# Kernel tuning notes

Measured on AMD Instinct MI355X. Metric: run time of the kernel, lower is better.

Reference implementation:

```python
import jax, jax.numpy as jnp
import numpy as np

SEQ, B, D_IN, D_TRAJ, D_LSTM = 640, 40, 8, 32, 64
NH, DH = 4, 48  # n_head, att_out
EMB = NH * DH  # 192


def setup_inputs() -> dict:
    key = jax.random.key(0)
    ks = jax.random.split(key, 16)
    g = lambda k, shape: (jax.random.normal(k, shape, dtype=jnp.float32) * 0.05)
    z = lambda n: jnp.zeros((n,), jnp.float32)
    return {
        "hist": jax.random.normal(ks[0], (128, 5, 40, D_IN), dtype=jnp.float32),
        "adj": jnp.zeros((B, B), dtype=jnp.int32),  # unused (use_spatial=False)
        "W1": g(ks[1], (D_TRAJ, D_IN)), "b1": z(D_TRAJ),
        "W_ih": g(ks[2], (4 * D_LSTM, D_TRAJ)), "W_hh": g(ks[3], (4 * D_LSTM, D_LSTM)),
        "b_ih": z(4 * D_LSTM), "b_hh": z(4 * D_LSTM),
        "Wq": g(ks[4], (EMB, D_LSTM)), "bq": z(EMB),
        "Wk": g(ks[5], (EMB, D_LSTM)), "bk": z(EMB),
        "Wv": g(ks[6], (EMB, D_LSTM)), "bv": z(EMB),
        "Wa": g(ks[7], (D_LSTM, EMB)), "ba": z(D_LSTM),
        "Wg": g(ks[8], (D_LSTM, EMB)), "bg": z(D_LSTM),
        "gamma": jnp.ones((D_LSTM,), jnp.float32), "beta": z(D_LSTM),
    }


def reference(hist, adj, W1, b1, W_ih, W_hh, b_ih, b_hh,
              Wq, bq, Wk, bk, Wv, bv, Wa, ba, Wg, bg, gamma, beta):
    # trajectory embedding + ELU
    x = jax.nn.elu(jnp.einsum('...f,hf->...h', hist, W1) + b1)
    x = x.reshape(SEQ, B, D_TRAJ)  # hardcoded (128*5, 40, 32) in the module

    # single-layer LSTM (torch gate order i, f, g, o), seq-first
    def step(carry, xt):
        h, c = carry
        gates = xt @ W_ih.T + h @ W_hh.T + b_ih + b_hh
        i, f, g_, o = jnp.split(gates, 4, axis=-1)
        c = jax.nn.sigmoid(f) * c + jax.nn.sigmoid(i) * jnp.tanh(g_)
        h = jax.nn.sigmoid(o) * jnp.tanh(c)
        return (h, c), h

    h0 = jnp.zeros((B, D_LSTM), x.dtype)
    (_, _), seq = jax.lax.scan(step, (h0, h0), x)  # (640, 40, 64)

    # multi-head attention over the 40-agent axis, per time step
    def heads(W, b):
        y = seq @ W.T + b  # (640, 40, 192)
        return y.reshape(SEQ, B, NH, DH).transpose(2, 0, 1, 3)  # (4, 640, 40, 48)

    q, k, v = heads(Wq, bq), heads(Wk, bk), heads(Wv, bv)
    a = jax.nn.softmax(jnp.einsum('hnqd,hnkd->hnqk', q, k) / 8.0, axis=-1)  # /sqrt(64)
    o = jnp.einsum('hnqk,hnkd->hnqd', a, v)  # (4, 640, 40, 48)
    o = o.transpose(1, 2, 0, 3).reshape(SEQ, B, EMB)  # recombine heads -> (640, 40, 192)

    # GLU (dropout rate = 0)
    tv = (o @ Wa.T + ba) * jax.nn.sigmoid(o @ Wg.T + bg)  # (640, 40, 64)

    # Add & LayerNorm (residual with LSTM output)
    y = seq + tv
    mu = y.mean(-1, keepdims=True)
    var = ((y - mu) ** 2).mean(-1, keepdims=True)
    return (y - mu) / jnp.sqrt(var + 1e-5) * gamma + beta
```

## Files before the change

kernel.cpp:

```cpp
#include <hip/hip_runtime.h>

#define SEQ 640
#define BATCH 40
#define D_IN 8
#define D_TRAJ 32
#define D_LSTM 64
#define G4 256
#define NH 4
#define DH 48
#define EMB 192

typedef float v2f __attribute__((ext_vector_type(2)));
typedef float v4f __attribute__((ext_vector_type(4)));
typedef _Float16 h2t __attribute__((ext_vector_type(2)));

__device__ __forceinline__ float sigmoid_f(float x) {
    float e = __expf(-x);
    return __builtin_amdgcn_rcpf(1.f + e);
}
__device__ __forceinline__ float tanh_f(float x) {
    float e = __expf(2.f * x);
    return 1.f - 2.f * __builtin_amdgcn_rcpf(e + 1.f);
}

__global__ void __launch_bounds__(256) k_embed(
    const float* __restrict__ hist, const float* __restrict__ W1,
    const float* __restrict__ b1, const float* __restrict__ W_ih,
    const float* __restrict__ b_ih, const float* __restrict__ b_hh,
    float* __restrict__ gates_x)
{
    __shared__ float sh_hist[BATCH * D_IN];
    __shared__ float sh_traj[BATCH * D_TRAJ];
    const int t = blockIdx.x, tid = threadIdx.x;

    for (int i = tid; i < BATCH * D_IN; i += 256)
        sh_hist[i] = hist[t * BATCH * D_IN + i];
    __syncthreads();

    for (int idx = tid; idx < BATCH * D_TRAJ; idx += 256) {
        int b = idx >> 5, h = idx & 31;
        float acc = b1[h];
        #pragma unroll
        for (int f = 0; f < D_IN; ++f)
            acc += sh_hist[b * D_IN + f] * W1[h * D_IN + f];
        sh_traj[idx] = acc > 0.f ? acc : (__expf(acc) - 1.f);
    }
    __syncthreads();

    float w[D_TRAJ];
    #pragma unroll
    for (int h = 0; h < D_TRAJ; ++h) w[h] = W_ih[tid * D_TRAJ + h];
    const float bias = b_ih[tid] + b_hh[tid];
    const int j = tid & 63, g = tid >> 6;

    for (int b = 0; b < BATCH; ++b) {
        float acc = bias;
        #pragma unroll
        for (int h = 0; h < D_TRAJ; ++h)
            acc += sh_traj[b * D_TRAJ + h] * w[h];
        gates_x[((size_t)b * SEQ + t) * G4 + j * 4 + g] = acc;
    }
}

__global__ void __launch_bounds__(64, 1) k_lstm(
    const float* __restrict__ gates_x, const float* __restrict__ W_hh,
    float* __restrict__ seq_out)
{
    const int b = blockIdx.x, j = threadIdx.x;

    h2t wi2[32], wf2[32], wg2[32], wo2[32];
    const float* Wi = W_hh + (0 * 64 + j) * D_LSTM;
    const float* Wf = W_hh + (1 * 64 + j) * D_LSTM;
    const float* Wg = W_hh + (2 * 64 + j) * D_LSTM;
    const float* Wo = W_hh + (3 * 64 + j) * D_LSTM;
    #pragma unroll
    for (int m = 0; m < 32; ++m) {
        wi2[m] = (h2t){(_Float16)Wi[2 * m], (_Float16)Wi[2 * m + 1]};
        wf2[m] = (h2t){(_Float16)Wf[2 * m], (_Float16)Wf[2 * m + 1]};
        wg2[m] = (h2t){(_Float16)Wg[2 * m], (_Float16)Wg[2 * m + 1]};
        wo2[m] = (h2t){(_Float16)Wo[2 * m], (_Float16)Wo[2 * m + 1]};
    }

    const v4f* gxp = (const v4f*)(gates_x + (size_t)b * SEQ * G4);
    v4f g0 = gxp[0 * 64 + j];
    v4f g1 = gxp[1 * 64 + j];
    v4f g2 = gxp[2 * 64 + j];
    v4f g3 = gxp[3 * 64 + j];

    float h = 0.f, c = 0.f;
    float hpf = 0.f;

    auto lstm_step = [&](v4f& gk, int t) {
        const int hbits = __builtin_bit_cast(int, hpf);

        float ai0 = gk.x, af0 = gk.y, ag0 = gk.z, ao0 = gk.w;
        float ai1 = 0.f, af1 = 0.f, ag1 = 0.f, ao1 = 0.f;
        #pragma unroll
        for (int m = 0; m < 16; ++m) {
            int pmi = __builtin_amdgcn_readlane(hbits, 2 * m);
            h2t p = __builtin_bit_cast(h2t, pmi);
            ai0 = __builtin_amdgcn_fdot2(wi2[m], p, ai0, false);
            af0 = __builtin_amdgcn_fdot2(wf2[m], p, af0, false);
            ag0 = __builtin_amdgcn_fdot2(wg2[m], p, ag0, false);
            ao0 = __builtin_amdgcn_fdot2(wo2[m], p, ao0, false);
        }
        #pragma unroll
        for (int m = 16; m < 32; ++m) {
            int pmi = __builtin_amdgcn_readlane(hbits, 2 * m);
            h2t p = __builtin_bit_cast(h2t, pmi);
            ai1 = __builtin_amdgcn_fdot2(wi2[m], p, ai1, false);
            af1 = __builtin_amdgcn_fdot2(wf2[m], p, af1, false);
            ag1 = __builtin_amdgcn_fdot2(wg2[m], p, ag1, false);
            ao1 = __builtin_amdgcn_fdot2(wo2[m], p, ao1, false);
        }
        float ai = ai0 + ai1, af = af0 + af1, ag = ag0 + ag1, ao = ao0 + ao1;

        c = sigmoid_f(af) * c + sigmoid_f(ai) * tanh_f(ag);
        h = sigmoid_f(ao) * tanh_f(c);
        seq_out[(size_t)(t * BATCH + b) * D_LSTM + j] = h;

        float hn = __shfl_xor(h, 1, 64);
        float lo = (j & 1) ? hn : h;
        float hi = (j & 1) ? h : hn;
        h2t hpk = {(_Float16)lo, (_Float16)hi};
        hpf = __builtin_bit_cast(float, hpk);

        int tp = t + 4; if (tp > SEQ - 1) tp = SEQ - 1;
        gk = gxp[(size_t)tp * 64 + j];
    };

    for (int t = 0; t < SEQ; t += 4) {
        lstm_step(g0, t + 0);
        lstm_step(g1, t + 1);
        lstm_step(g2, t + 2);
        lstm_step(g3, t + 3);
    }
}

__global__ void __launch_bounds__(256) k_wtrans(
    const float* __restrict__ Wq, const float* __restrict__ bq,
    const float* __restrict__ Wk, const float* __restrict__ bk,
    const float* __restrict__ Wv, const float* __restrict__ bv,
    float* __restrict__ WT, float* __restrict__ bqkv)
{
    int idx = blockIdx.x * 256 + threadIdx.x;
    if (idx < 576 * 64) {
        int k = idx / 576, c = idx % 576;
        float v;
        if (c < 192)      v = Wq[c * 64 + k];
        else if (c < 384) v = Wk[(c - 192) * 64 + k];
        else              v = Wv[(c - 384) * 64 + k];
        WT[idx] = v;
    }
    if (idx < 576) {
        float v;
        if (idx < 192)      v = bq[idx];
        else if (idx < 384) v = bk[idx - 192];
        else                v = bv[idx - 384];
        bqkv[idx] = v;
    }
}

#define QKVS 584
#define SXS 68
#define SSS 44
__global__ void __launch_bounds__(256) k_attn(
    const float* __restrict__ seq, const float* __restrict__ WT,
    const float* __restrict__ bqkv, float* __restrict__ o_buf)
{
    const int t = blockIdx.x, tid = threadIdx.x;
    __shared__ _Float16 sqkv[BATCH * QKVS];
    __shared__ float sX[BATCH * SXS];

    for (int i = tid; i < BATCH * D_LSTM; i += 256)
        sX[(i >> 6) * SXS + (i & 63)] = seq[(size_t)t * BATCH * D_LSTM + i];
    __syncthreads();

    const int c0 = tid, c1 = tid + 256, c2 = tid + 512;
    const float b0v = bqkv[c0], b1v = bqkv[c1];
    const float b2v = (tid < 64) ? bqkv[c2] : 0.f;

    for (int grp = 0; grp < 2; ++grp) {
        float a0[20], a1[20], a2[20];
        #pragma unroll
        for (int r = 0; r < 20; ++r) { a0[r] = b0v; a1[r] = b1v; a2[r] = b2v; }

        for (int kq = 0; kq < 16; ++kq) {
            float w0[4], w1[4], w2[4];
            #pragma unroll
            for (int u = 0; u < 4; ++u) {
                int k = 4 * kq + u;
                w0[u] = WT[k * 576 + c0];
                w1[u] = WT[k * 576 + c1];
                w2[u] = (tid < 64) ? WT[k * 576 + c2] : 0.f;
            }
            #pragma unroll
            for (int r = 0; r < 20; ++r) {
                v4f x = *(const v4f*)&sX[(grp * 20 + r) * SXS + 4 * kq];
                a0[r] += x.x * w0[0] + x.y * w0[1] + x.z * w0[2] + x.w * w0[3];
                a1[r] += x.x * w1[0] + x.y * w1[1] + x.z * w1[2] + x.w * w1[3];
                a2[r] += x.x * w2[0] + x.y * w2[1] + x.z * w2[2] + x.w * w2[3];
            }
        }
        for (int r = 0; r < 20; ++r) {
            int bb = grp * 20 + r;
            sqkv[bb * QKVS + c0] = (_Float16)a0[r];
            sqkv[bb * QKVS + c1] = (_Float16)a1[r];
            if (tid < 64) sqkv[bb * QKVS + c2] = (_Float16)a2[r];
        }
    }
    __syncthreads();

    float* ss = sX;

    for (int h = 0; h < NH; ++h) {
        for (int p = 0; p < 2; ++p) {
            if (tid < 200) {
                int slot = p * 200 + tid;
                int i = slot / 10, jg = slot % 10;
                const v4f* qp = (const v4f*)&sqkv[i * QKVS + h * DH];
                v4f q[6];
                #pragma unroll
                for (int u = 0; u < 6; ++u) q[u] = qp[u];
                #pragma unroll
                for (int v = 0; v < 4; ++v) {
                    int jj = jg * 4 + v;
                    const v4f* kp = (const v4f*)&sqkv[jj * QKVS + 192 + h * DH];
                    float acc = 0.f;
                    #pragma unroll
                    for (int u = 0; u < 6; ++u) {
                        v4f kv = kp[u];
                        acc = __builtin_amdgcn_fdot2(
                            __builtin_bit_cast(h2t, q[u].x),
                            __builtin_bit_cast(h2t, kv.x), acc, false);
                        acc = __builtin_amdgcn_fdot2(
                            __builtin_bit_cast(h2t, q[u].y),
                            __builtin_bit_cast(h2t, kv.y), acc, false);
                        acc = __builtin_amdgcn_fdot2(
                            __builtin_bit_cast(h2t, q[u].z),
                            __builtin_bit_cast(h2t, kv.z), acc, false);
                        acc = __builtin_amdgcn_fdot2(
                            __builtin_bit_cast(h2t, q[u].w),
                            __builtin_bit_cast(h2t, kv.w), acc, false);
                    }
                    ss[i * SSS + jj] = acc * 0.125f;
                }
            }
        }
        __syncthreads();

        if (tid < BATCH) {
            v4f* rp = (v4f*)&ss[tid * SSS];
            v4f r[10];
            #pragma unroll
            for (int u = 0; u < 10; ++u) r[u] = rp[u];
            float m = -1e30f;
            #pragma unroll
            for (int u = 0; u < 10; ++u)
                m = fmaxf(m, fmaxf(fmaxf(r[u].x, r[u].y), fmaxf(r[u].z, r[u].w)));
            float s = 0.f;
            #pragma unroll
            for (int u = 0; u < 10; ++u) {
                r[u].x = __expf(r[u].x - m); s += r[u].x;
                r[u].y = __expf(r[u].y - m); s += r[u].y;
                r[u].z = __expf(r[u].z - m); s += r[u].z;
                r[u].w = __expf(r[u].w - m); s += r[u].w;
            }
            float inv = __builtin_amdgcn_rcpf(s);
            #pragma unroll
            for (int u = 0; u < 10; ++u) {
                r[u].x *= inv; r[u].y *= inv; r[u].z *= inv; r[u].w *= inv;
                rp[u] = r[u];
            }
        }
        __syncthreads();

        if (tid < 240) {
            int bi = tid / 6, dg = tid % 6, d0 = dg * 8;
            const v4f* sp = (const v4f*)&ss[bi * SSS];
            v4f sr[10];
            #pragma unroll
            for (int u = 0; u < 10; ++u) sr[u] = sp[u];
            float acc[8];
            #pragma unroll
            for (int d = 0; d < 8; ++d) acc[d] = 0.f;
            for (int jj = 0; jj < 40; ++jj) {
                float a = ((const float*)&sr[jj >> 2])[jj & 3];
                v4f vv = *(const v4f*)&sqkv[jj * QKVS + 384 + h * DH + d0];
                #pragma unroll
                for (int w = 0; w < 4; ++w) {
                    h2t pr = __builtin_bit_cast(h2t, ((const float*)&vv)[w]);
                    acc[2 * w]     += a * (float)pr[0];
                    acc[2 * w + 1] += a * (float)pr[1];
                }
            }
            float* ob = &o_buf[((size_t)t * BATCH + bi) * EMB + h * DH + d0];
            #pragma unroll
            for (int d = 0; d < 8; ++d) ob[d] = acc[d];
        }
        __syncthreads();
    }
}

__global__ void __launch_bounds__(256) k_glu_ln(
    const float* __restrict__ seq, const float* __restrict__ obuf,
    const float* __restrict__ Wa, const float* __restrict__ ba,
    const float* __restrict__ Wg, const float* __restrict__ bg,
    const float* __restrict__ gamma, const float* __restrict__ beta,
    float* __restrict__ out)
{
    const int t = blockIdx.x, tid = threadIdx.x;
    __shared__ float so[BATCH * 193];
    __shared__ float sy[BATCH * 65];
    __shared__ float sseq[BATCH * D_LSTM];

    const float* ot = obuf + (size_t)t * BATCH * EMB;
    for (int i = tid; i < BATCH * EMB; i += 256)
        so[(i / EMB) * 193 + (i % EMB)] = ot[i];
    for (int i = tid; i < BATCH * D_LSTM; i += 256)
        sseq[i] = seq[(size_t)t * BATCH * D_LSTM + i];
    __syncthreads();

    const int j = tid >> 2, bgr = tid & 3;
    float acc_a[10], acc_g[10];
    #pragma unroll
    for (int bb = 0; bb < 10; ++bb) { acc_a[bb] = ba[j]; acc_g[bb] = bg[j]; }

    const float* wa = Wa + j * EMB;
    const float* wg = Wg + j * EMB;
    for (int p = 0; p < EMB; ++p) {
        float a = wa[p], g = wg[p];
        #pragma unroll
        for (int bb = 0; bb < 10; ++bb) {
            float o = so[(bgr + 4 * bb) * 193 + p];
            acc_a[bb] += o * a;
            acc_g[bb] += o * g;
        }
    }
    #pragma unroll
    for (int bb = 0; bb < 10; ++bb) {
        int b = bgr + 4 * bb;
        float tv = acc_a[bb] * sigmoid_f(acc_g[bb]);
        sy[b * 65 + j] = sseq[b * D_LSTM + j] + tv;
    }
    __syncthreads();

    const int w = tid >> 6, lane = tid & 63;
    const float gm = gamma[lane], bt = beta[lane];
    for (int rr = 0; rr < 10; ++rr) {
        int b = w + 4 * rr;
        float y = sy[b * 65 + lane];
        float s1 = y, s2 = y * y;
        #pragma unroll
        for (int m = 1; m < 64; m <<= 1) {
            s1 += __shfl_xor(s1, m, 64);
            s2 += __shfl_xor(s2, m, 64);
        }
        float mu  = s1 * (1.f / 64.f);
        float var = s2 * (1.f / 64.f) - mu * mu;
        float inv = rsqrtf(var + 1e-5f);
        out[(size_t)t * BATCH * D_LSTM + b * D_LSTM + lane] = (y - mu) * inv * gm + bt;
    }
}

extern "C" void kernel_launch(void* const* d_in, const int* in_sizes, int n_in,
                              void* d_out, int out_size, void* d_ws, size_t ws_size,
                              hipStream_t stream)
{
    const float* hist = (const float*)d_in[0];
    const float* W1   = (const float*)d_in[2];
    const float* b1   = (const float*)d_in[3];
    const float* W_ih = (const float*)d_in[4];
    const float* W_hh = (const float*)d_in[5];
    const float* b_ih = (const float*)d_in[6];
    const float* b_hh = (const float*)d_in[7];
    const float* Wq   = (const float*)d_in[8];
    const float* bq   = (const float*)d_in[9];
    const float* Wk   = (const float*)d_in[10];
    const float* bk   = (const float*)d_in[11];
    const float* Wv   = (const float*)d_in[12];
    const float* bv   = (const float*)d_in[13];
    const float* Wa   = (const float*)d_in[14];
    const float* ba   = (const float*)d_in[15];
    const float* Wg   = (const float*)d_in[16];
    const float* bg   = (const float*)d_in[17];
    const float* gamma = (const float*)d_in[18];
    const float* beta  = (const float*)d_in[19];
    float* out = (float*)d_out;

    float* ws = (float*)d_ws;
    float* gates_x = ws;
    float* seq     = ws + 6553600;
    float* obuf    = ws + 6553600 + 1638400;
    float* WT      = ws + 6553600 + 1638400 + 4915200;
    float* bqkv    = WT + 36864;

    hipLaunchKernelGGL(k_wtrans, dim3(144), dim3(256), 0, stream,
                       Wq, bq, Wk, bk, Wv, bv, WT, bqkv);
    hipLaunchKernelGGL(k_embed, dim3(SEQ), dim3(256), 0, stream,
                       hist, W1, b1, W_ih, b_ih, b_hh, gates_x);
    hipLaunchKernelGGL(k_lstm, dim3(BATCH), dim3(64), 0, stream,
                       gates_x, W_hh, seq);
    hipLaunchKernelGGL(k_attn, dim3(SEQ), dim3(256), 0, stream,
                       seq, WT, bqkv, obuf);
    hipLaunchKernelGGL(k_glu_ln, dim3(SEQ), dim3(256), 0, stream,
                       seq, obuf, Wa, ba, Wg, bg, gamma, beta, out);
}
```

Before: 513.1 us.

## Fuse attention with GLU+LayerNorm and use DPP for LSTM hidden-state exchange

Merges the attention and GLU/LayerNorm kernels so each head's output stays in shared memory and is folded into GLU accumulators right away, which removes the o_buf global round trip and one launch. The LSTM's recurrent h exchange swaps a shuffle for a DPP quad-permute of packed fp16 halves, shortening the serial per-step critical path. W_ih loads in the embed kernel become vectorized. The cost is more registers and shared memory in the fused kernel, which may lower occupancy, and the LSTM chain is still the dominant serial part.

```diff
diff --git a/kernel.cpp b/kernel.cpp
--- a/kernel.cpp
+++ b/kernel.cpp
@@ -48,8 +48,14 @@
     __syncthreads();
 
     float w[D_TRAJ];
-    #pragma unroll
-    for (int h = 0; h < D_TRAJ; ++h) w[h] = W_ih[tid * D_TRAJ + h];
+    {
+        const v4f* wv = (const v4f*)(W_ih + tid * D_TRAJ);
+        #pragma unroll
+        for (int u = 0; u < 8; ++u) {
+            v4f x = wv[u];
+            w[4*u] = x.x; w[4*u+1] = x.y; w[4*u+2] = x.z; w[4*u+3] = x.w;
+        }
+    }
     const float bias = b_ih[tid] + b_hh[tid];
     const int j = tid & 63, g = tid >> 6;
 
@@ -89,6 +95,7 @@
 
     float h = 0.f, c = 0.f;
     float hpf = 0.f;
+    const bool odd = (j & 1);
 
     auto lstm_step = [&](v4f& gk, int t) {
         const int hbits = __builtin_bit_cast(int, hpf);
@@ -119,11 +126,10 @@
         h = sigmoid_f(ao) * tanh_f(c);
         seq_out[(size_t)(t * BATCH + b) * D_LSTM + j] = h;
 
-        float hn = __shfl_xor(h, 1, 64);
-        float lo = (j & 1) ? hn : h;
-        float hi = (j & 1) ? h : hn;
-        h2t hpk = {(_Float16)lo, (_Float16)hi};
-        hpf = __builtin_bit_cast(float, hpk);
+        int own = (int)__builtin_bit_cast(unsigned short, (_Float16)h);
+        int nb  = __builtin_amdgcn_update_dpp(0, own, 0xB1, 0xF, 0xF, true);
+        int pk  = odd ? (nb | (own << 16)) : (own | (nb << 16));
+        hpf = __builtin_bit_cast(float, pk);
 
         int tp = t + 4; if (tp > SEQ - 1) tp = SEQ - 1;
         gk = gxp[(size_t)tp * 64 + j];
@@ -164,13 +170,18 @@
 #define QKVS 584
 #define SXS 68
 #define SSS 44
-__global__ void __launch_bounds__(256) k_attn(
+#define SOS 52
+__global__ void __launch_bounds__(256, 2) k_attn_glu(
     const float* __restrict__ seq, const float* __restrict__ WT,
-    const float* __restrict__ bqkv, float* __restrict__ o_buf)
+    const float* __restrict__ bqkv,
+    const float* __restrict__ Wa, const float* __restrict__ ba,
+    const float* __restrict__ Wg, const float* __restrict__ bg,
+    const float* __restrict__ gamma, const float* __restrict__ beta,
+    float* __restrict__ out)
 {
     const int t = blockIdx.x, tid = threadIdx.x;
     __shared__ _Float16 sqkv[BATCH * QKVS];
-    __shared__ float sX[BATCH * SXS];
+    __shared__ float sX[5280];
 
     for (int i = tid; i < BATCH * D_LSTM; i += 256)
         sX[(i >> 6) * SXS + (i & 63)] = seq[(size_t)t * BATCH * D_LSTM + i];
@@ -212,6 +223,12 @@
     __syncthreads();
 
     float* ss = sX;
+    float* so = sX + 2720;
+
+    const int gj = tid >> 2, bgr = tid & 3;
+    float acc_a[10], acc_g[10];
+    #pragma unroll
+    for (int bb = 0; bb < 10; ++bb) { acc_a[bb] = ba[gj]; acc_g[bb] = bg[gj]; }
 
     for (int h = 0; h < NH; ++h) {
         for (int p = 0; p < 2; ++p) {
@@ -294,72 +311,58 @@
                     acc[2 * w + 1] += a * (float)pr[1];
                 }
             }
-            float* ob = &o_buf[((size_t)t * BATCH + bi) * EMB + h * DH + d0];
-            #pragma unroll
-            for (int d = 0; d < 8; ++d) ob[d] = acc[d];
+            v4f* op = (v4f*)&so[bi * SOS + d0];
+            op[0] = (v4f){acc[0], acc[1], acc[2], acc[3]};
+            op[1] = (v4f){acc[4], acc[5], acc[6], acc[7]};
         }
         __syncthreads();
-    }
-}
-
-__global__ void __launch_bounds__(256) k_glu_ln(
-    const float* __restrict__ seq, const float* __restrict__ obuf,
-    const float* __restrict__ Wa, const float* __restrict__ ba,
-    const float* __restrict__ Wg, const float* __restrict__ bg,
-    const float* __restrict__ gamma, const float* __restrict__ beta,
-    float* __restrict__ out)
-{
-    const int t = blockIdx.x, tid = threadIdx.x;
-    __shared__ float so[BATCH * 193];
-    __shared__ float sy[BATCH * 65];
-    __shared__ float sseq[BATCH * D_LSTM];
-
-    const float* ot = obuf + (size_t)t * BATCH * EMB;
-    for (int i = tid; i < BATCH * EMB; i += 256)
-        so[(i / EMB) * 193 + (i % EMB)] = ot[i];
+
+        {
+            const v4f* wap = (const v4f*)(Wa + gj * EMB + h * DH);
+            const v4f* wgp = (const v4f*)(Wg + gj * EMB + h * DH);
+            for (int pc = 0; pc < 12; ++pc) {
+                v4f a4 = wap[pc], g4 = wgp[pc];
+                #pragma unroll
+                for (int bb = 0; bb < 10; ++bb) {
+                    v4f ov = *(const v4f*)&so[(bgr + 4 * bb) * SOS + 4 * pc];
+                    acc_a[bb] += ov.x * a4.x + ov.y * a4.y + ov.z * a4.z + ov.w * a4.w;
+                    acc_g[bb] += ov.x * g4.x + ov.y * g4.y + ov.z * g4.z + ov.w * g4.w;
+                }
+            }
+        }
+    }
+
     for (int i = tid; i < BATCH * D_LSTM; i += 256)
-        sseq[i] = seq[(size_t)t * BATCH * D_LSTM + i];
-    __syncthreads();
-
-    const int j = tid >> 2, bgr = tid & 3;
-    float acc_a[10], acc_g[10];
-    #pragma unroll
-    for (int bb = 0; bb < 10; ++bb) { acc_a[bb] = ba[j]; acc_g[bb] = bg[j]; }
-
-    const float* wa = Wa + j * EMB;
-    const float* wg = Wg + j * EMB;
-    for (int p = 0; p < EMB; ++p) {
-        float a = wa[p], g = wg[p];
-        #pragma unroll
-        for (int bb = 0; bb < 10; ++bb) {
-            float o = so[(bgr + 4 * bb) * 193 + p];
-            acc_a[bb] += o * a;
-            acc_g[bb] += o * g;
-        }
-    }
+        sX[i] = seq[(size_t)t * BATCH * D_LSTM + i];
+    __syncthreads();
+
+    float* sy = sX + 2680;
     #pragma unroll
     for (int bb = 0; bb < 10; ++bb) {
         int b = bgr + 4 * bb;
         float tv = acc_a[bb] * sigmoid_f(acc_g[bb]);
-        sy[b * 65 + j] = sseq[b * D_LSTM + j] + tv;
-    }
-    __syncthreads();
-
-    const int w = tid >> 6, lane = tid & 63;
-    const float gm = gamma[lane], bt = beta[lane];
-    for (int rr = 0; rr < 10; ++rr) {
-        int b = w + 4 * rr;
-        float y = sy[b * 65 + lane];
-        float s1 = y, s2 = y * y;
-        #pragma unroll
-        for (int m = 1; m < 64; m <<= 1) {
-            s1 += __shfl_xor(s1, m, 64);
-            s2 += __shfl_xor(s2, m, 64);
-        }
-        float mu  = s1 * (1.f / 64.f);
-        float var = s2 * (1.f / 64.f) - mu * mu;
-        float inv = rsqrtf(var + 1e-5f);
-        out[(size_t)t * BATCH * D_LSTM + b * D_LSTM + lane] = (y - mu) * inv * gm + bt;
+        sy[b * 65 + gj] = sX[b * D_LSTM + gj] + tv;
+    }
+    __syncthreads();
+
+    {
+        const int w = tid >> 6, lane = tid & 63;
+        const float gm = gamma[lane], bt = beta[lane];
+        for (int rr = 0; rr < 10; ++rr) {
+            int b = w + 4 * rr;
+            float y = sy[b * 65 + lane];
+            float s1 = y, s2 = y * y;
+            #pragma unroll
+            for (int m = 1; m < 64; m <<= 1) {
+                s1 += __shfl_xor(s1, m, 64);
+                s2 += __shfl_xor(s2, m, 64);
+            }
+            float mu  = s1 * (1.f / 64.f);
+            float var = s2 * (1.f / 64.f) - mu * mu;
+            float inv = rsqrtf(var + 1e-5f);
+            out[(size_t)t * BATCH * D_LSTM + b * D_LSTM + lane] =
+                (y - mu) * inv * gm + bt;
+        }
     }
 }
 
@@ -391,8 +394,7 @@
     float* ws = (float*)d_ws;
     float* gates_x = ws;
     float* seq     = ws + 6553600;
-    float* obuf    = ws + 6553600 + 1638400;
-    float* WT      = ws + 6553600 + 1638400 + 4915200;
+    float* WT      = ws + 6553600 + 1638400;
     float* bqkv    = WT + 36864;
 
     hipLaunchKernelGGL(k_wtrans, dim3(144), dim3(256), 0, stream,
@@ -401,8 +403,6 @@
                        hist, W1, b1, W_ih, b_ih, b_hh, gates_x);
     hipLaunchKernelGGL(k_lstm, dim3(BATCH), dim3(64), 0, stream,
                        gates_x, W_hh, seq);
-    hipLaunchKernelGGL(k_attn, dim3(SEQ), dim3(256), 0, stream,
-                       seq, WT, bqkv, obuf);
-    hipLaunchKernelGGL(k_glu_ln, dim3(SEQ), dim3(256), 0, stream,
-                       seq, obuf, Wa, ba, Wg, bg, gamma, beta, out);
-}
+    hipLaunchKernelGGL(k_attn_glu, dim3(SEQ), dim3(256), 0, stream,
+                       seq, WT, bqkv, Wa, ba, Wg, bg, gamma, beta, out);
+}
```

Result: faster. 502.6 us (-2.1%).

## Split attention per head across blocks, drop weight-transpose kernel, use DPP in LSTM

Applied to the files above, without the earlier changes.

The attention kernel now launches one block per (head, timestep) instead of one per timestep. Each block computes only its head's Q/K/V projection, with 144 threads each holding a 64-wide weight row in registers loaded straight from the original weights. This removes the separate transpose kernel and the serial per-head loop, and gives four times more blocks. The cost is that the seq tile is loaded four times and 112 threads sit idle during projection. The LSTM neighbour exchange swaps a shuffle for a DPP quad-permute on packed fp16 bits, and the embed kernel loads W_ih with vector loads.

```diff
diff --git a/kernel.cpp b/kernel.cpp
--- a/kernel.cpp
+++ b/kernel.cpp
@@ -48,8 +48,14 @@
     __syncthreads();
 
     float w[D_TRAJ];
-    #pragma unroll
-    for (int h = 0; h < D_TRAJ; ++h) w[h] = W_ih[tid * D_TRAJ + h];
+    {
+        const v4f* wv = (const v4f*)(W_ih + tid * D_TRAJ);
+        #pragma unroll
+        for (int u = 0; u < 8; ++u) {
+            v4f x = wv[u];
+            w[4*u] = x.x; w[4*u+1] = x.y; w[4*u+2] = x.z; w[4*u+3] = x.w;
+        }
+    }
     const float bias = b_ih[tid] + b_hh[tid];
     const int j = tid & 63, g = tid >> 6;
 
@@ -89,6 +95,7 @@
 
     float h = 0.f, c = 0.f;
     float hpf = 0.f;
+    const bool odd = (j & 1);
 
     auto lstm_step = [&](v4f& gk, int t) {
         const int hbits = __builtin_bit_cast(int, hpf);
@@ -119,11 +126,10 @@
         h = sigmoid_f(ao) * tanh_f(c);
         seq_out[(size_t)(t * BATCH + b) * D_LSTM + j] = h;
 
-        float hn = __shfl_xor(h, 1, 64);
-        float lo = (j & 1) ? hn : h;
-        float hi = (j & 1) ? h : hn;
-        h2t hpk = {(_Float16)lo, (_Float16)hi};
-        hpf = __builtin_bit_cast(float, hpk);
+        int own = (int)__builtin_bit_cast(unsigned short, (_Float16)h);
+        int nb  = __builtin_amdgcn_update_dpp(0, own, 0xB1, 0xF, 0xF, true);
+        int pk  = odd ? (nb | (own << 16)) : (own | (nb << 16));
+        hpf = __builtin_bit_cast(float, pk);
 
         int tp = t + 4; if (tp > SEQ - 1) tp = SEQ - 1;
         gk = gxp[(size_t)tp * 64 + j];
@@ -137,168 +143,125 @@
     }
 }
 
-__global__ void __launch_bounds__(256) k_wtrans(
+#define SAS 68
+#define SKVS 152
+#define SSS 44
+__global__ void __launch_bounds__(256) k_attn(
+    const float* __restrict__ seq,
     const float* __restrict__ Wq, const float* __restrict__ bq,
     const float* __restrict__ Wk, const float* __restrict__ bk,
     const float* __restrict__ Wv, const float* __restrict__ bv,
-    float* __restrict__ WT, float* __restrict__ bqkv)
-{
-    int idx = blockIdx.x * 256 + threadIdx.x;
-    if (idx < 576 * 64) {
-        int k = idx / 576, c = idx % 576;
-        float v;
-        if (c < 192)      v = Wq[c * 64 + k];
-        else if (c < 384) v = Wk[(c - 192) * 64 + k];
-        else              v = Wv[(c - 384) * 64 + k];
-        WT[idx] = v;
-    }
-    if (idx < 576) {
-        float v;
-        if (idx < 192)      v = bq[idx];
-        else if (idx < 384) v = bk[idx - 192];
-        else                v = bv[idx - 384];
-        bqkv[idx] = v;
-    }
-}
-
-#define QKVS 584
-#define SXS 68
-#define SSS 44
-__global__ void __launch_bounds__(256) k_attn(
-    const float* __restrict__ seq, const float* __restrict__ WT,
-    const float* __restrict__ bqkv, float* __restrict__ o_buf)
-{
-    const int t = blockIdx.x, tid = threadIdx.x;
-    __shared__ _Float16 sqkv[BATCH * QKVS];
-    __shared__ float sX[BATCH * SXS];
+    float* __restrict__ o_buf)
+{
+    const int h = blockIdx.x, t = blockIdx.y, tid = threadIdx.x;
+    __shared__ float sA[BATCH * SAS];
+    __shared__ _Float16 skqv[BATCH * SKVS];
+    __shared__ float ss[BATCH * SSS];
 
     for (int i = tid; i < BATCH * D_LSTM; i += 256)
-        sX[(i >> 6) * SXS + (i & 63)] = seq[(size_t)t * BATCH * D_LSTM + i];
-    __syncthreads();
-
-    const int c0 = tid, c1 = tid + 256, c2 = tid + 512;
-    const float b0v = bqkv[c0], b1v = bqkv[c1];
-    const float b2v = (tid < 64) ? bqkv[c2] : 0.f;
-
-    for (int grp = 0; grp < 2; ++grp) {
-        float a0[20], a1[20], a2[20];
-        #pragma unroll
-        for (int r = 0; r < 20; ++r) { a0[r] = b0v; a1[r] = b1v; a2[r] = b2v; }
-
-        for (int kq = 0; kq < 16; ++kq) {
-            float w0[4], w1[4], w2[4];
+        sA[(i >> 6) * SAS + (i & 63)] = seq[(size_t)t * BATCH * D_LSTM + i];
+    __syncthreads();
+
+    if (tid < 144) {
+        int m = tid / 48, d = tid - m * 48;
+        const float* W = (m == 0) ? Wq : (m == 1) ? Wk : Wv;
+        const float* B = (m == 0) ? bq : (m == 1) ? bk : bv;
+        const float* wrow = W + (h * DH + d) * D_LSTM;
+        float wreg[D_LSTM];
+        {
+            const v4f* wv = (const v4f*)wrow;
             #pragma unroll
-            for (int u = 0; u < 4; ++u) {
-                int k = 4 * kq + u;
-                w0[u] = WT[k * 576 + c0];
-                w1[u] = WT[k * 576 + c1];
-                w2[u] = (tid < 64) ? WT[k * 576 + c2] : 0.f;
+            for (int u = 0; u < 16; ++u) {
+                v4f x = wv[u];
+                wreg[4*u] = x.x; wreg[4*u+1] = x.y;
+                wreg[4*u+2] = x.z; wreg[4*u+3] = x.w;
             }
+        }
+        const float bias = B[h * DH + d];
+
+        for (int a = 0; a < BATCH; ++a) {
+            const v4f* ap = (const v4f*)&sA[a * SAS];
+            float acc = bias;
             #pragma unroll
-            for (int r = 0; r < 20; ++r) {
-                v4f x = *(const v4f*)&sX[(grp * 20 + r) * SXS + 4 * kq];
-                a0[r] += x.x * w0[0] + x.y * w0[1] + x.z * w0[2] + x.w * w0[3];
-                a1[r] += x.x * w1[0] + x.y * w1[1] + x.z * w1[2] + x.w * w1[3];
-                a2[r] += x.x * w2[0] + x.y * w2[1] + x.z * w2[2] + x.w * w2[3];
+            for (int u = 0; u < 16; ++u) {
+                v4f av = ap[u];
+                acc += av.x * wreg[4*u]   + av.y * wreg[4*u+1]
+                     + av.z * wreg[4*u+2] + av.w * wreg[4*u+3];
             }
-        }
-        for (int r = 0; r < 20; ++r) {
-            int bb = grp * 20 + r;
-            sqkv[bb * QKVS + c0] = (_Float16)a0[r];
-            sqkv[bb * QKVS + c1] = (_Float16)a1[r];
-            if (tid < 64) sqkv[bb * QKVS + c2] = (_Float16)a2[r];
-        }
-    }
-    __syncthreads();
-
-    float* ss = sX;
-
-    for (int h = 0; h < NH; ++h) {
-        for (int p = 0; p < 2; ++p) {
-            if (tid < 200) {
-                int slot = p * 200 + tid;
-                int i = slot / 10, jg = slot % 10;
-                const v4f* qp = (const v4f*)&sqkv[i * QKVS + h * DH];
-                v4f q[6];
-                #pragma unroll
-                for (int u = 0; u < 6; ++u) q[u] = qp[u];
-                #pragma unroll
-                for (int v = 0; v < 4; ++v) {
-                    int jj = jg * 4 + v;
-                    const v4f* kp = (const v4f*)&sqkv[jj * QKVS + 192 + h * DH];
-                    float acc = 0.f;
-                    #pragma unroll
-                    for (int u = 0; u < 6; ++u) {
-                        v4f kv = kp[u];
-                        acc = __builtin_amdgcn_fdot2(
-                            __builtin_bit_cast(h2t, q[u].x),
-                            __builtin_bit_cast(h2t, kv.x), acc, false);
-                        acc = __builtin_amdgcn_fdot2(
-                            __builtin_bit_cast(h2t, q[u].y),
-                            __builtin_bit_cast(h2t, kv.y), acc, false);
-                        acc = __builtin_amdgcn_fdot2(
-                            __builtin_bit_cast(h2t, q[u].z),
-                            __builtin_bit_cast(h2t, kv.z), acc, false);
-                        acc = __builtin_amdgcn_fdot2(
-                            __builtin_bit_cast(h2t, q[u].w),
-                            __builtin_bit_cast(h2t, kv.w), acc, false);
-                    }
-                    ss[i * SSS + jj] = acc * 0.125f;
-                }
+            skqv[a * SKVS + tid] = (_Float16)acc;
+        }
+    }
+    __syncthreads();
+
+    for (int idx = tid; idx < BATCH * BATCH; idx += 256) {
+        int i = idx / BATCH, jj = idx % BATCH;
+        const v4f* qp = (const v4f*)&skqv[i * SKVS];
+        const v4f* kp = (const v4f*)&skqv[jj * SKVS + 48];
+        float acc = 0.f;
+        #pragma unroll
+        for (int u = 0; u < 6; ++u) {
+            v4f qv = qp[u], kv = kp[u];
+            acc = __builtin_amdgcn_fdot2(__builtin_bit_cast(h2t, qv.x),
+                    __builtin_bit_cast(h2t, kv.x), acc, false);
+            acc = __builtin_amdgcn_fdot2(__builtin_bit_cast(h2t, qv.y),
+                    __builtin_bit_cast(h2t, kv.y), acc, false);
+            acc = __builtin_amdgcn_fdot2(__builtin_bit_cast(h2t, qv.z),
+                    __builtin_bit_cast(h2t, kv.z), acc, false);
+            acc = __builtin_amdgcn_fdot2(__builtin_bit_cast(h2t, qv.w),
+                    __builtin_bit_cast(h2t, kv.w), acc, false);
+        }
+        ss[i * SSS + jj] = acc * 0.125f;
+    }
+    __syncthreads();
+
+    if (tid < BATCH) {
+        v4f* rp = (v4f*)&ss[tid * SSS];
+        v4f r[10];
+        #pragma unroll
+        for (int u = 0; u < 10; ++u) r[u] = rp[u];
+        float m = -1e30f;
+        #pragma unroll
+        for (int u = 0; u < 10; ++u)
+            m = fmaxf(m, fmaxf(fmaxf(r[u].x, r[u].y), fmaxf(r[u].z, r[u].w)));
+        float s = 0.f;
+        #pragma unroll
+        for (int u = 0; u < 10; ++u) {
+            r[u].x = __expf(r[u].x - m); s += r[u].x;
+            r[u].y = __expf(r[u].y - m); s += r[u].y;
+            r[u].z = __expf(r[u].z - m); s += r[u].z;
+            r[u].w = __expf(r[u].w - m); s += r[u].w;
+        }
+        float inv = __builtin_amdgcn_rcpf(s);
+        #pragma unroll
+        for (int u = 0; u < 10; ++u) {
+            r[u].x *= inv; r[u].y *= inv; r[u].z *= inv; r[u].w *= inv;
+            rp[u] = r[u];
+        }
+    }
+    __syncthreads();
+
+    if (tid < 240) {
+        int bi = tid / 6, dg = tid % 6, d0 = dg * 8;
+        const v4f* sp = (const v4f*)&ss[bi * SSS];
+        v4f sr[10];
+        #pragma unroll
+        for (int u = 0; u < 10; ++u) sr[u] = sp[u];
+        float acc[8];
+        #pragma unroll
+        for (int d = 0; d < 8; ++d) acc[d] = 0.f;
+        for (int jj = 0; jj < 40; ++jj) {
+            float a = ((const float*)&sr[jj >> 2])[jj & 3];
+            v4f vv = *(const v4f*)&skqv[jj * SKVS + 96 + d0];
+            #pragma unroll
+            for (int w = 0; w < 4; ++w) {
+                h2t pr = __builtin_bit_cast(h2t, ((const float*)&vv)[w]);
+                acc[2 * w]     += a * (float)pr[0];
+                acc[2 * w + 1] += a * (float)pr[1];
             }
         }
-        __syncthreads();
-
-        if (tid < BATCH) {
-            v4f* rp = (v4f*)&ss[tid * SSS];
-            v4f r[10];
-            #pragma unroll
-            for (int u = 0; u < 10; ++u) r[u] = rp[u];
-            float m = -1e30f;
-            #pragma unroll
-            for (int u = 0; u < 10; ++u)
-                m = fmaxf(m, fmaxf(fmaxf(r[u].x, r[u].y), fmaxf(r[u].z, r[u].w)));
-            float s = 0.f;
-            #pragma unroll
-            for (int u = 0; u < 10; ++u) {
-                r[u].x = __expf(r[u].x - m); s += r[u].x;
-                r[u].y = __expf(r[u].y - m); s += r[u].y;
-                r[u].z = __expf(r[u].z - m); s += r[u].z;
-                r[u].w = __expf(r[u].w - m); s += r[u].w;
-            }
-            float inv = __builtin_amdgcn_rcpf(s);
-            #pragma unroll
-            for (int u = 0; u < 10; ++u) {
-                r[u].x *= inv; r[u].y *= inv; r[u].z *= inv; r[u].w *= inv;
-                rp[u] = r[u];
-            }
-        }
-        __syncthreads();
-
-        if (tid < 240) {
-            int bi = tid / 6, dg = tid % 6, d0 = dg * 8;
-            const v4f* sp = (const v4f*)&ss[bi * SSS];
-            v4f sr[10];
-            #pragma unroll
-            for (int u = 0; u < 10; ++u) sr[u] = sp[u];
-            float acc[8];
-            #pragma unroll
-            for (int d = 0; d < 8; ++d) acc[d] = 0.f;
-            for (int jj = 0; jj < 40; ++jj) {
-                float a = ((const float*)&sr[jj >> 2])[jj & 3];
-                v4f vv = *(const v4f*)&sqkv[jj * QKVS + 384 + h * DH + d0];
-                #pragma unroll
-                for (int w = 0; w < 4; ++w) {
-                    h2t pr = __builtin_bit_cast(h2t, ((const float*)&vv)[w]);
-                    acc[2 * w]     += a * (float)pr[0];
-                    acc[2 * w + 1] += a * (float)pr[1];
-                }
-            }
-            float* ob = &o_buf[((size_t)t * BATCH + bi) * EMB + h * DH + d0];
-            #pragma unroll
-            for (int d = 0; d < 8; ++d) ob[d] = acc[d];
-        }
-        __syncthreads();
+        float* ob = &o_buf[((size_t)t * BATCH + bi) * EMB + h * DH + d0];
+        *(v4f*)&ob[0] = (v4f){acc[0], acc[1], acc[2], acc[3]};
+        *(v4f*)&ob[4] = (v4f){acc[4], acc[5], acc[6], acc[7]};
     }
 }
 
@@ -359,7 +322,8 @@
         float mu  = s1 * (1.f / 64.f);
         float var = s2 * (1.f / 64.f) - mu * mu;
         float inv = rsqrtf(var + 1e-5f);
-        out[(size_t)t * BATCH * D_LSTM + b * D_LSTM + lane] = (y - mu) * inv * gm + bt;
+        out[(size_t)t * BATCH * D_LSTM + b * D_LSTM + lane] =
+            (y - mu) * inv * gm + bt;
     }
 }
 
@@ -392,17 +356,13 @@
     float* gates_x = ws;
     float* seq     = ws + 6553600;
     float* obuf    = ws + 6553600 + 1638400;
-    float* WT      = ws + 6553600 + 1638400 + 4915200;
-    float* bqkv    = WT + 36864;
-
-    hipLaunchKernelGGL(k_wtrans, dim3(144), dim3(256), 0, stream,
-                       Wq, bq, Wk, bk, Wv, bv, WT, bqkv);
+
     hipLaunchKernelGGL(k_embed, dim3(SEQ), dim3(256), 0, stream,
                        hist, W1, b1, W_ih, b_ih, b_hh, gates_x);
     hipLaunchKernelGGL(k_lstm, dim3(BATCH), dim3(64), 0, stream,
                        gates_x, W_hh, seq);
-    hipLaunchKernelGGL(k_attn, dim3(SEQ), dim3(256), 0, stream,
-                       seq, WT, bqkv, obuf);
+    hipLaunchKernelGGL(k_attn, dim3(NH, SEQ), dim3(256), 0, stream,
+                       seq, Wq, bq, Wk, bk, Wv, bv, obuf);
     hipLaunchKernelGGL(k_glu_ln, dim3(SEQ), dim3(256), 0, stream,
                        seq, obuf, Wa, ba, Wg, bg, gamma, beta, out);
 }
```

Measured after the change: 495.7 us. 1.04x faster.
